# Kernel optimization log

Hardware: AMD Instinct MI355X
Metric: run time of the kernel (lower is better)

The kernel has to match this reference:

```python
import jax, jax.numpy as jnp
import numpy as np
from jax import lax

F = 64          # nb_filters
K_DOWN = 4      # size_kernel_sample
K_RES = 3       # size_kernel_res
DIL = 3         # rate_dilation_res
N_DOWN = 3      # downsampling blocks (one level)
N_RES = 4       # residual sub-blocks per block
N_EMB = 512     # codebook size
BETA = 0.25


def conv1d(x, w, b, stride=1, dil=1, act=True):
    # x: (B,T,C), w: (K,Cin,Cout)
    y = lax.conv_general_dilated(x, w, (stride,), 'SAME', rhs_dilation=(dil,),
                                 dimension_numbers=('NWC', 'WIO', 'NWC')) + b
    return jax.nn.relu(y) if act else y


def conv1d_t(x, w, b, stride):
    # transposed conv, w: (K, Cin, Cout)
    y = lax.conv_transpose(x, w, (stride,), 'SAME',
                           dimension_numbers=('NWC', 'WIO', 'NWC')) + b
    return jax.nn.relu(y)


def setup_inputs() -> dict:
    key = jax.random.key(0)
    ks = jax.random.split(key, 12)
    s_in = 1.0 / np.sqrt(K_DOWN * 1)
    s_f = 1.0 / np.sqrt(K_DOWN * F)
    s_r = 1.0 / np.sqrt(K_RES * F)
    return {
        'x': jax.random.normal(ks[0], (4, 65536, 1), dtype=jnp.float32),
        'w_down0': jax.random.normal(ks[1], (K_DOWN, 1, F), dtype=jnp.float32) * s_in,
        'b_down0': jnp.zeros((F,), jnp.float32),
        'w_down': jax.random.normal(ks[2], (N_DOWN - 1, K_DOWN, F, F), dtype=jnp.float32) * s_f,
        'b_down': jnp.zeros((N_DOWN - 1, F), jnp.float32),
        'w_res_enc': jax.random.normal(ks[3], (N_DOWN, N_RES, 2, K_RES, F, F), dtype=jnp.float32) * s_r,
        'b_res_enc': jnp.zeros((N_DOWN, N_RES, 2, F), jnp.float32),
        'codebook': jax.random.normal(ks[4], (N_EMB, F), dtype=jnp.float32),
        'w_res_dec': jax.random.normal(ks[5], (N_DOWN, N_RES, 2, K_RES, F, F), dtype=jnp.float32) * s_r,
        'b_res_dec': jnp.zeros((N_DOWN, N_RES, 2, F), jnp.float32),
        'w_up': jax.random.normal(ks[6], (N_DOWN, K_DOWN, F, F), dtype=jnp.float32) * s_f,
        'b_up': jnp.zeros((N_DOWN, F), jnp.float32),
        'w_proj': jax.random.normal(ks[7], (K_RES, F, 1), dtype=jnp.float32) * s_r,
        'b_proj': jnp.zeros((1,), jnp.float32),
    }


def reference(x, w_down0, b_down0, w_down, b_down, w_res_enc, b_res_enc,
              codebook, w_res_dec, b_res_dec, w_up, b_up, w_proj, b_proj):
    # ---- Encoder: N_DOWN stride-2 downsampling blocks, each followed by
    # N_RES ForwardResidualSubBlocks (dilated conv -> conv, residual add) ----
    h = conv1d(x, w_down0, b_down0, stride=2)
    for blk in range(N_DOWN):
        if blk > 0:
            h = conv1d(h, w_down[blk - 1], b_down[blk - 1], stride=2)
        for r in range(N_RES):
            y = conv1d(h, w_res_enc[blk, r, 0], b_res_enc[blk, r, 0], dil=DIL)
            y = conv1d(y, w_res_enc[blk, r, 1], b_res_enc[blk, r, 1], dil=1)
            h = h + y
    z_e = h  # (B, T/8, F)

    # ---- VectorQuantiser over channel axis ----
    dot = jnp.einsum('btd,kd->btk', z_e, codebook)          # tensordot
    nz = jnp.sum(jnp.square(z_e), axis=-1, keepdims=True)   # (B,T,1)
    ne = jnp.sum(jnp.square(codebook), axis=-1)             # (K,)
    dist = -2.0 * dot + nz + ne                             # squared cdist
    ids = jnp.argmin(dist, axis=-1)                         # (B,T)
    z_q = codebook[ids]                                     # embedding_lookup
    loss_commit = jnp.mean(jnp.linalg.norm(lax.stop_gradient(z_e) - z_q, axis=-1))
    loss_codebook = jnp.mean(jnp.linalg.norm(z_e - lax.stop_gradient(z_q), axis=-1))
    loss_vq = loss_codebook + BETA * loss_commit
    similarity = dot / jnp.sqrt(nz) / jnp.sqrt(ne)

    # ---- Decoder: residual blocks then stride-2 transposed conv, x N_DOWN ----
    h = z_q
    for blk in range(N_DOWN):
        for r in range(N_RES):
            y = conv1d(h, w_res_dec[blk, r, 0], b_res_dec[blk, r, 0], dil=1)
            y = conv1d(y, w_res_dec[blk, r, 1], b_res_dec[blk, r, 1], dil=DIL)
            h = h + y
        h = conv1d_t(h, w_up[blk], b_up[blk], stride=2)
    x_hat = conv1d(h, w_proj, b_proj, act=False)  # linear projection
    return x_hat, loss_vq, ids, similarity
```

## Files before the change

kernel.cpp:

```cpp
#include <hip/hip_runtime.h>
#include <cstdint>


#define OFF_LOSS 262144
#define OFF_IDS  262145
#define OFF_SIM  294913

__global__ __launch_bounds__(256) void down0_kernel(
    const float* __restrict__ x, const float* __restrict__ w,
    const float* __restrict__ bias, float* __restrict__ y)
{
  int idx = blockIdx.x * 256 + threadIdx.x;
  int co = idx & 63;
  int r  = idx >> 6;
  int t  = r & 32767;
  int b  = r >> 15;
  const float* xb = x + (size_t)b * 65536;
  float acc = bias[co];
  #pragma unroll
  for (int k = 0; k < 4; ++k) {
    int gt = 2 * t - 1 + k;
    float xv = ((unsigned)gt < 65536u) ? xb[gt] : 0.f;
    acc += xv * w[k * 64 + co];
  }
  y[(size_t)idx] = fmaxf(acc, 0.f);
}

template <int DIL, bool HAS_RES, int TT>
__global__ __launch_bounds__(512, 8) void conv3_kernel(
    const float* __restrict__ x, const float* __restrict__ w,
    const float* __restrict__ bias, const float* res,
    float* y, int T)
{
  constexpr int TPL = TT / 64;
  constexpr int XT  = TT + 2 * DIL;
  constexpr int XS0 = (XT + 3) & ~3;
  constexpr int XS  = (XS0 % 8 == 4) ? XS0 : XS0 + 4;
  constexpr int NV  = TPL + 2 * DIL;
  __shared__ float xs[64 * XS];
  const int tid  = threadIdx.x;
  const int lane = tid & 63;
  const int b    = blockIdx.y;
  const int t0   = blockIdx.x * TT;
  const int wv   = __builtin_amdgcn_readfirstlane(tid >> 6);
  const int co0  = __builtin_amdgcn_readfirstlane(wv * 8);

  const float* xb = x + (size_t)b * T * 64;
  for (int e = tid; e < 16 * XT; e += 512) {
    int tl = e >> 4, cq = (e & 15) * 4;
    int gt = t0 - DIL + tl;
    float4 v = make_float4(0.f, 0.f, 0.f, 0.f);
    if ((unsigned)gt < (unsigned)T) v = *(const float4*)&xb[(size_t)gt * 64 + cq];
    xs[(cq + 0) * XS + tl] = v.x;
    xs[(cq + 1) * XS + tl] = v.y;
    xs[(cq + 2) * XS + tl] = v.z;
    xs[(cq + 3) * XS + tl] = v.w;
  }
  __syncthreads();

  float acc[TPL][8] = {};
  const float* wb = w + co0;
  const int tb = TPL * lane;
  for (int ci = 0; ci < 64; ++ci) {
    const float* xr = xs + ci * XS + tb;
    float xv[NV];
    if constexpr (TPL == 2) {
      const float2* p2 = (const float2*)xr;
      #pragma unroll
      for (int q = 0; q < NV / 2; ++q) { float2 v = p2[q]; xv[2*q] = v.x; xv[2*q+1] = v.y; }
    } else {
      #pragma unroll
      for (int j = 0; j < NV; ++j) xv[j] = xr[j];
    }
    const float* w0 = wb + (0 * 64 + ci) * 64;
    const float* w1 = wb + (1 * 64 + ci) * 64;
    const float* w2 = wb + (2 * 64 + ci) * 64;
    #pragma unroll
    for (int j = 0; j < 8; ++j) {
      float c0 = w0[j], c1 = w1[j], c2 = w2[j];
      #pragma unroll
      for (int i = 0; i < TPL; ++i)
        acc[i][j] = fmaf(xv[i], c0, fmaf(xv[i + DIL], c1, fmaf(xv[i + 2 * DIL], c2, acc[i][j])));
    }
  }

  float bs[8];
  #pragma unroll
  for (int j = 0; j < 8; ++j) bs[j] = bias[co0 + j];
  #pragma unroll
  for (int i = 0; i < TPL; ++i) {
    size_t o = ((size_t)b * T + t0 + tb + i) * 64 + co0;
    float r[8];
    #pragma unroll
    for (int j = 0; j < 8; ++j) r[j] = fmaxf(acc[i][j] + bs[j], 0.f);
    if (HAS_RES) {
      float4 v0 = *(const float4*)&res[o];
      float4 v1 = *(const float4*)&res[o + 4];
      r[0] += v0.x; r[1] += v0.y; r[2] += v0.z; r[3] += v0.w;
      r[4] += v1.x; r[5] += v1.y; r[6] += v1.z; r[7] += v1.w;
    }
    *(float4*)&y[o]     = make_float4(r[0], r[1], r[2], r[3]);
    *(float4*)&y[o + 4] = make_float4(r[4], r[5], r[6], r[7]);
  }
}

__global__ __launch_bounds__(512, 8) void down2_kernel(
    const float* __restrict__ x, const float* __restrict__ w,
    const float* __restrict__ bias, float* __restrict__ y, int Tin)
{
  constexpr int XT = 130, XS = 132;
  __shared__ float xs[64 * XS];
  const int tid  = threadIdx.x;
  const int lane = tid & 63;
  const int b    = blockIdx.y;
  const int t0   = blockIdx.x * 64;
  const int Tout = Tin >> 1;
  const int wv   = __builtin_amdgcn_readfirstlane(tid >> 6);
  const int co0  = __builtin_amdgcn_readfirstlane(wv * 8);

  const float* xb = x + (size_t)b * Tin * 64;
  for (int e = tid; e < 16 * XT; e += 512) {
    int tl = e >> 4, cq = (e & 15) * 4;
    int gt = 2 * t0 - 1 + tl;
    float4 v = make_float4(0.f, 0.f, 0.f, 0.f);
    if ((unsigned)gt < (unsigned)Tin) v = *(const float4*)&xb[(size_t)gt * 64 + cq];
    xs[(cq + 0) * XS + tl] = v.x;
    xs[(cq + 1) * XS + tl] = v.y;
    xs[(cq + 2) * XS + tl] = v.z;
    xs[(cq + 3) * XS + tl] = v.w;
  }
  __syncthreads();

  float acc[8] = {};
  const float* wb = w + co0;
  for (int ci = 0; ci < 64; ++ci) {
    const float2* p2 = (const float2*)(xs + ci * XS + 2 * lane);
    float2 v0 = p2[0], v1 = p2[1];
    float a0 = v0.x, a1 = v0.y, a2 = v1.x, a3 = v1.y;
    const float* w0 = wb + (0 * 64 + ci) * 64;
    const float* w1 = wb + (1 * 64 + ci) * 64;
    const float* w2 = wb + (2 * 64 + ci) * 64;
    const float* w3 = wb + (3 * 64 + ci) * 64;
    #pragma unroll
    for (int j = 0; j < 8; ++j)
      acc[j] = fmaf(a0, w0[j], fmaf(a1, w1[j], fmaf(a2, w2[j], fmaf(a3, w3[j], acc[j]))));
  }

  size_t o = ((size_t)b * Tout + t0 + lane) * 64 + co0;
  #pragma unroll
  for (int q = 0; q < 2; ++q) {
    float4 rr;
    rr.x = fmaxf(acc[4*q+0] + bias[co0 + 4*q+0], 0.f);
    rr.y = fmaxf(acc[4*q+1] + bias[co0 + 4*q+1], 0.f);
    rr.z = fmaxf(acc[4*q+2] + bias[co0 + 4*q+2], 0.f);
    rr.w = fmaxf(acc[4*q+3] + bias[co0 + 4*q+3], 0.f);
    *(float4*)&y[o + 4 * q] = rr;
  }
}

__global__ __launch_bounds__(512, 8) void up_kernel(
    const float* __restrict__ x, const float* __restrict__ w,
    const float* __restrict__ bias, float* __restrict__ y, int Tin)
{
  constexpr int XT = 66, XS = 68;
  __shared__ float xs[64 * XS];
  const int tid  = threadIdx.x;
  const int lane = tid & 63;
  const int b    = blockIdx.y;
  const int u0   = blockIdx.x * 64;
  const int Tout = Tin << 1;
  const int wv   = __builtin_amdgcn_readfirstlane(tid >> 6);
  const int co0  = __builtin_amdgcn_readfirstlane(wv * 8);

  const float* xb = x + (size_t)b * Tin * 64;
  for (int e = tid; e < 16 * XT; e += 512) {
    int ul = e >> 4, cq = (e & 15) * 4;
    int gu = u0 - 1 + ul;
    float4 v = make_float4(0.f, 0.f, 0.f, 0.f);
    if ((unsigned)gu < (unsigned)Tin) v = *(const float4*)&xb[(size_t)gu * 64 + cq];
    xs[(cq + 0) * XS + ul] = v.x;
    xs[(cq + 1) * XS + ul] = v.y;
    xs[(cq + 2) * XS + ul] = v.z;
    xs[(cq + 3) * XS + ul] = v.w;
  }
  __syncthreads();

  float acce[8] = {}, acco[8] = {};
  const float* wb = w + co0;
  for (int ci = 0; ci < 64; ++ci) {
    const float* xr = xs + ci * XS + lane;
    float a0 = xr[0], a1 = xr[1], a2 = xr[2];
    const float* w0 = wb + (0 * 64 + ci) * 64;
    const float* w1 = wb + (1 * 64 + ci) * 64;
    const float* w2 = wb + (2 * 64 + ci) * 64;
    const float* w3 = wb + (3 * 64 + ci) * 64;
    #pragma unroll
    for (int j = 0; j < 8; ++j) {
      acce[j] = fmaf(a0, w0[j], fmaf(a1, w2[j], acce[j]));
      acco[j] = fmaf(a1, w1[j], fmaf(a2, w3[j], acco[j]));
    }
  }

  size_t oe = ((size_t)b * Tout + 2 * (u0 + lane)) * 64 + co0;
  size_t oo = oe + 64;
  #pragma unroll
  for (int q = 0; q < 2; ++q) {
    float4 re, ro;
    re.x = fmaxf(acce[4*q+0] + bias[co0 + 4*q+0], 0.f);
    re.y = fmaxf(acce[4*q+1] + bias[co0 + 4*q+1], 0.f);
    re.z = fmaxf(acce[4*q+2] + bias[co0 + 4*q+2], 0.f);
    re.w = fmaxf(acce[4*q+3] + bias[co0 + 4*q+3], 0.f);
    ro.x = fmaxf(acco[4*q+0] + bias[co0 + 4*q+0], 0.f);
    ro.y = fmaxf(acco[4*q+1] + bias[co0 + 4*q+1], 0.f);
    ro.z = fmaxf(acco[4*q+2] + bias[co0 + 4*q+2], 0.f);
    ro.w = fmaxf(acco[4*q+3] + bias[co0 + 4*q+3], 0.f);
    *(float4*)&y[oe + 4 * q] = re;
    *(float4*)&y[oo + 4 * q] = ro;
  }
}

__global__ __launch_bounds__(256) void proj_kernel(
    const float* __restrict__ x, const float* __restrict__ w,
    const float* __restrict__ bias, float* __restrict__ out)
{
  const int lane = threadIdx.x & 63;
  const int wid  = (blockIdx.x * 256 + threadIdx.x) >> 6;
  const float w0 = w[lane], w1 = w[64 + lane], w2 = w[128 + lane];
  const float bb = bias[0];
  size_t base = (size_t)wid * 64;
  for (int i = 0; i < 64; ++i) {
    size_t tau = base + i;
    int b = (int)(tau >> 16);
    int t = (int)(tau & 65535);
    const float* xb = x + ((size_t)b * 65536) * 64;
    float pm = (t > 0)     ? xb[(size_t)(t - 1) * 64 + lane] : 0.f;
    float pc =               xb[(size_t)t * 64 + lane];
    float pp = (t < 65535) ? xb[(size_t)(t + 1) * 64 + lane] : 0.f;
    float s = pm * w0 + pc * w1 + pp * w2;
    #pragma unroll
    for (int off = 32; off; off >>= 1) s += __shfl_down(s, off);
    if (lane == 0) out[tau] = s + bb;
  }
}

__global__ __launch_bounds__(256) void nz_kernel(
    const float* __restrict__ ze, float* __restrict__ nz)
{
  int lane = threadIdx.x & 63;
  int tok  = (blockIdx.x * 256 + threadIdx.x) >> 6;
  float v = ze[(size_t)tok * 64 + lane];
  float s = v * v;
  #pragma unroll
  for (int off = 32; off; off >>= 1) s += __shfl_down(s, off);
  if (lane == 0) nz[tok] = s;
}

#define VQA_TOKS 32
__global__ __launch_bounds__(256) void vq_dots_kernel(
    const float* __restrict__ ze, const float* __restrict__ cb,
    const float* __restrict__ nzbuf, float* __restrict__ sim_out,
    float2* __restrict__ pmin)
{
  __shared__ float zs[VQA_TOKS * 64];
  const int tid = threadIdx.x;
  {
    const float4* src = (const float4*)(ze + (size_t)blockIdx.x * VQA_TOKS * 64);
    float4* dst = (float4*)zs;
    dst[tid]       = src[tid];
    dst[tid + 256] = src[tid + 256];
  }
  const int c = blockIdx.y * 256 + tid;
  float r[64];
  #pragma unroll
  for (int q = 0; q < 16; ++q) {
    float4 a = ((const float4*)cb)[(size_t)c * 16 + q];
    r[4*q] = a.x; r[4*q+1] = a.y; r[4*q+2] = a.z; r[4*q+3] = a.w;
  }
  float ne = 0.f;
  #pragma unroll
  for (int d = 0; d < 64; ++d) ne += r[d] * r[d];
  const float rsne = 1.f / sqrtf(ne);
  const int wvid = tid >> 6;
  __syncthreads();

  for (int it = 0; it < VQA_TOKS; ++it) {
    const int tok = blockIdx.x * VQA_TOKS + it;
    const float4* z4 = (const float4*)(zs + it * 64);
    float dot = 0.f;
    #pragma unroll
    for (int q = 0; q < 16; ++q) {
      float4 zv = z4[q];
      dot += zv.x * r[4*q] + zv.y * r[4*q+1] + zv.z * r[4*q+2] + zv.w * r[4*q+3];
    }
    const float nzv = nzbuf[tok];
    float dist = (-2.f * dot + nzv) + ne;
    sim_out[(size_t)tok * 512 + c] = dot * (1.f / sqrtf(nzv)) * rsne;

    float md = dist; int mi = c;
    #pragma unroll
    for (int off = 32; off; off >>= 1) {
      float od = __shfl_down(md, off);
      int   oi = __shfl_down(mi, off);
      if (od < md || (od == md && oi < mi)) { md = od; mi = oi; }
    }
    if ((tid & 63) == 0) pmin[tok * 8 + blockIdx.y * 4 + wvid] = make_float2(md, (float)mi);
  }
}

__global__ __launch_bounds__(256) void vq_finish_kernel(
    const float* __restrict__ ze, const float* __restrict__ cb,
    const float2* __restrict__ pmin, float* __restrict__ zq,
    float* __restrict__ ids_out, float* __restrict__ blocksum)
{
  const int tid = threadIdx.x;
  const int lane = tid & 63, wvid = tid >> 6;
  float lloss = 0.f;
  for (int it = 0; it < 16; ++it) {
    const int tok = blockIdx.x * 64 + wvid * 16 + it;
    float bd = 1e30f; int bi = 0;
    #pragma unroll
    for (int p = 0; p < 8; ++p) {
      float2 pr = pmin[tok * 8 + p];
      float d = pr.x; int i = (int)pr.y;
      if (d < bd || (d == bd && i < bi)) { bd = d; bi = i; }
    }
    float zev = ze[(size_t)tok * 64 + lane];
    float cv  = cb[(size_t)bi * 64 + lane];
    float df = zev - cv;
    float s = df * df;
    #pragma unroll
    for (int off = 32; off; off >>= 1) s += __shfl_down(s, off);
    zq[(size_t)tok * 64 + lane] = cv;
    if (lane == 0) { ids_out[tok] = (float)bi; lloss += sqrtf(s); }
  }
  __shared__ float ls[4];
  if (lane == 0) ls[wvid] = lloss;
  __syncthreads();
  if (tid == 0) blocksum[blockIdx.x] = ls[0] + ls[1] + ls[2] + ls[3];
}

__global__ void loss_fin_kernel(const float* __restrict__ blocksum,
                                float* __restrict__ out)
{
  const int lane = threadIdx.x;
  float s = 0.f;
  for (int i = lane; i < 512; i += 64) s += blocksum[i];
  #pragma unroll
  for (int off = 32; off; off >>= 1) s += __shfl_down(s, off);
  if (lane == 0) out[0] = 1.25f * s / 32768.f;
}

#define LAUNCH_CONV3(DILV, RESV, XP, WP, BP, RP, YP)                           \
  do {                                                                         \
    if (T >= 16384)                                                            \
      conv3_kernel<DILV, RESV, 128><<<dim3(T / 128, 4), 512, 0, stream>>>(     \
          XP, WP, BP, RP, YP, T);                                              \
    else                                                                       \
      conv3_kernel<DILV, RESV, 64><<<dim3(T / 64, 4), 512, 0, stream>>>(       \
          XP, WP, BP, RP, YP, T);                                              \
  } while (0)

extern "C" void kernel_launch(void* const* d_in, const int* in_sizes, int n_in,
                              void* d_out, int out_size, void* d_ws, size_t ws_size,
                              hipStream_t stream)
{
  const float* x       = (const float*)d_in[0];
  const float* w_down0 = (const float*)d_in[1];
  const float* b_down0 = (const float*)d_in[2];
  const float* w_down  = (const float*)d_in[3];
  const float* b_down  = (const float*)d_in[4];
  const float* w_res_e = (const float*)d_in[5];
  const float* b_res_e = (const float*)d_in[6];
  const float* cb      = (const float*)d_in[7];
  const float* w_res_d = (const float*)d_in[8];
  const float* b_res_d = (const float*)d_in[9];
  const float* w_up    = (const float*)d_in[10];
  const float* b_up    = (const float*)d_in[11];
  const float* w_proj  = (const float*)d_in[12];
  const float* b_proj  = (const float*)d_in[13];

  float* out = (float*)d_out;
  const size_t BUF = (size_t)4 * 65536 * 64;
  float*  bufA     = (float*)d_ws;
  float*  bufB     = bufA + BUF;
  float*  nzbuf    = bufB + BUF;
  float2* pmin     = (float2*)(nzbuf + 32768);
  float*  blocksum = (float*)(pmin + 32768 * 8);

  float* h = bufA;
  float* tmp = bufB;

  down0_kernel<<<32768, 256, 0, stream>>>(x, w_down0, b_down0, h);
  int T = 32768;
  for (int blk = 0; blk < 3; ++blk) {
    if (blk > 0) {
      down2_kernel<<<dim3(T / 2 / 64, 4), 512, 0, stream>>>(
          h, w_down + (size_t)(blk - 1) * 4 * 64 * 64, b_down + (blk - 1) * 64, tmp, T);
      T >>= 1;
      float* s = h; h = tmp; tmp = s;
    }
    for (int r = 0; r < 4; ++r) {
      const float* w0p = w_res_e + (((size_t)blk * 4 + r) * 2 + 0) * 3 * 64 * 64;
      const float* w1p = w_res_e + (((size_t)blk * 4 + r) * 2 + 1) * 3 * 64 * 64;
      const float* b0p = b_res_e + (((size_t)blk * 4 + r) * 2 + 0) * 64;
      const float* b1p = b_res_e + (((size_t)blk * 4 + r) * 2 + 1) * 64;
      LAUNCH_CONV3(3, false, h, w0p, b0p, nullptr, tmp);
      LAUNCH_CONV3(1, true,  tmp, w1p, b1p, h, h);
    }
  }

  nz_kernel<<<8192, 256, 0, stream>>>(h, nzbuf);
  vq_dots_kernel<<<dim3(32768 / VQA_TOKS, 2), 256, 0, stream>>>(h, cb, nzbuf, out + OFF_SIM, pmin);
  vq_finish_kernel<<<512, 256, 0, stream>>>(h, cb, pmin, tmp, out + OFF_IDS, blocksum);
  loss_fin_kernel<<<1, 64, 0, stream>>>(blocksum, out + OFF_LOSS);
  { float* s = h; h = tmp; tmp = s; }

  for (int blk = 0; blk < 3; ++blk) {
    for (int r = 0; r < 4; ++r) {
      const float* w0p = w_res_d + (((size_t)blk * 4 + r) * 2 + 0) * 3 * 64 * 64;
      const float* w1p = w_res_d + (((size_t)blk * 4 + r) * 2 + 1) * 3 * 64 * 64;
      const float* b0p = b_res_d + (((size_t)blk * 4 + r) * 2 + 0) * 64;
      const float* b1p = b_res_d + (((size_t)blk * 4 + r) * 2 + 1) * 64;
      LAUNCH_CONV3(1, false, h, w0p, b0p, nullptr, tmp);
      LAUNCH_CONV3(3, true,  tmp, w1p, b1p, h, h);
    }
    up_kernel<<<dim3(2 * T / 128, 4), 512, 0, stream>>>(
        h, w_up + (size_t)blk * 4 * 64 * 64, b_up + blk * 64, tmp, T);
    T <<= 1;
    float* s = h; h = tmp; tmp = s;
  }

  proj_kernel<<<1024, 256, 0, stream>>>(h, w_proj, b_proj, out);
}
```

Measured before the change: 1.744 ms.

## Restructure VQ dot kernel to stream codebook and keep per-token accumulators

The VQ distance kernel now streams each codebook row in 16-float chunks and accumulates dots for all 32 tokens in registers, instead of holding the full 64-float codebook row in registers and looping over tokens. The per-token argmin drops the paired value/index shuffle reduction in favour of an fminf xor-reduction followed by a ballot to find the lowest matching lane. A launch-bounds occupancy hint of 6 is added. The aim is lower register pressure, higher occupancy and fewer shuffle instructions. The cost is 32 live accumulators and a different reduction order for the dot products, which could change argmin ties in rare cases.

Result: slower. 3.717 ms (+113.1%).

```diff
diff --git a/kernel.cpp b/kernel.cpp
--- a/kernel.cpp
+++ b/kernel.cpp
@@ -256,7 +256,7 @@
 }
 
 #define VQA_TOKS 32
-__global__ __launch_bounds__(256) void vq_dots_kernel(
+__global__ __launch_bounds__(256, 6) void vq_dots_kernel(
     const float* __restrict__ ze, const float* __restrict__ cb,
     const float* __restrict__ nzbuf, float* __restrict__ sim_out,
     float2* __restrict__ pmin)
@@ -270,40 +270,57 @@
     dst[tid + 256] = src[tid + 256];
   }
   const int c = blockIdx.y * 256 + tid;
-  float r[64];
-  #pragma unroll
-  for (int q = 0; q < 16; ++q) {
-    float4 a = ((const float4*)cb)[(size_t)c * 16 + q];
-    r[4*q] = a.x; r[4*q+1] = a.y; r[4*q+2] = a.z; r[4*q+3] = a.w;
-  }
+  const float4* cb4 = (const float4*)(cb + (size_t)c * 64);
+  const int wvid = tid >> 6;
+
+  float acc[VQA_TOKS];
+  #pragma unroll
+  for (int t = 0; t < VQA_TOKS; ++t) acc[t] = 0.f;
   float ne = 0.f;
-  #pragma unroll
-  for (int d = 0; d < 64; ++d) ne += r[d] * r[d];
+  __syncthreads();
+
+  #pragma unroll
+  for (int q = 0; q < 4; ++q) {
+    float4 w0 = cb4[4 * q + 0];
+    float4 w1 = cb4[4 * q + 1];
+    float4 w2 = cb4[4 * q + 2];
+    float4 w3 = cb4[4 * q + 3];
+    ne += w0.x * w0.x + w0.y * w0.y + w0.z * w0.z + w0.w * w0.w
+        + w1.x * w1.x + w1.y * w1.y + w1.z * w1.z + w1.w * w1.w
+        + w2.x * w2.x + w2.y * w2.y + w2.z * w2.z + w2.w * w2.w
+        + w3.x * w3.x + w3.y * w3.y + w3.z * w3.z + w3.w * w3.w;
+    const float4* zq4 = (const float4*)(zs + q * 16);
+    #pragma unroll
+    for (int t = 0; t < VQA_TOKS; ++t) {
+      float4 z0 = zq4[t * 16 + 0];
+      float4 z1 = zq4[t * 16 + 1];
+      float4 z2 = zq4[t * 16 + 2];
+      float4 z3 = zq4[t * 16 + 3];
+      acc[t] += z0.x * w0.x + z0.y * w0.y + z0.z * w0.z + z0.w * w0.w
+              + z1.x * w1.x + z1.y * w1.y + z1.z * w1.z + z1.w * w1.w
+              + z2.x * w2.x + z2.y * w2.y + z2.z * w2.z + z2.w * w2.w
+              + z3.x * w3.x + z3.y * w3.y + z3.z * w3.z + z3.w * w3.w;
+    }
+  }
   const float rsne = 1.f / sqrtf(ne);
-  const int wvid = tid >> 6;
-  __syncthreads();
-
-  for (int it = 0; it < VQA_TOKS; ++it) {
-    const int tok = blockIdx.x * VQA_TOKS + it;
-    const float4* z4 = (const float4*)(zs + it * 64);
-    float dot = 0.f;
-    #pragma unroll
-    for (int q = 0; q < 16; ++q) {
-      float4 zv = z4[q];
-      dot += zv.x * r[4*q] + zv.y * r[4*q+1] + zv.z * r[4*q+2] + zv.w * r[4*q+3];
-    }
+  const int cbase = blockIdx.y * 256 + wvid * 64;
+
+  #pragma unroll
+  for (int t = 0; t < VQA_TOKS; ++t) {
+    const int tok = blockIdx.x * VQA_TOKS + t;
     const float nzv = nzbuf[tok];
-    float dist = (-2.f * dot + nzv) + ne;
+    const float dot = acc[t];
+    const float dist = (-2.f * dot + nzv) + ne;
     sim_out[(size_t)tok * 512 + c] = dot * (1.f / sqrtf(nzv)) * rsne;
 
-    float md = dist; int mi = c;
-    #pragma unroll
-    for (int off = 32; off; off >>= 1) {
-      float od = __shfl_down(md, off);
-      int   oi = __shfl_down(mi, off);
-      if (od < md || (od == md && oi < mi)) { md = od; mi = oi; }
-    }
-    if ((tid & 63) == 0) pmin[tok * 8 + blockIdx.y * 4 + wvid] = make_float2(md, (float)mi);
+    float md = dist;
+    #pragma unroll
+    for (int off = 32; off; off >>= 1) md = fminf(md, __shfl_xor(md, off));
+    unsigned long long mk = __ballot(dist == md);
+    if ((tid & 63) == 0) {
+      int lmin = __ffsll(mk) - 1;
+      pmin[tok * 8 + blockIdx.y * 4 + wvid] = make_float2(md, (float)(cbase + lmin));
+    }
   }
 }
 
```

## Rewrite VQ distance kernel as register-tiled shared-memory GEMM

Applied to the files above, without the earlier changes.

Replaces the per-thread codebook-row-in-registers VQ dot kernel with a 64-token by 128-entry tiled GEMM. Both operands are staged transposed in shared memory and each thread computes a 4x8 register tile. Codebook norms move to a separate small kernel, and partial argmin results drop from 8 to 4 per token. The aim is higher FMA-to-load reuse in the distance and similarity stage and vectorized similarity stores. In exchange it adds one tiny launch and more shared memory per block.

Result: faster. 1.626 ms (-6.8%).

```diff
diff --git a/kernel.cpp b/kernel.cpp
--- a/kernel.cpp
+++ b/kernel.cpp
@@ -255,55 +255,109 @@
   if (lane == 0) nz[tok] = s;
 }
 
-#define VQA_TOKS 32
+__global__ __launch_bounds__(256) void ne_kernel(
+    const float* __restrict__ cb, float* __restrict__ ne)
+{
+  int c = blockIdx.x * 256 + threadIdx.x;
+  const float4* p = (const float4*)(cb + (size_t)c * 64);
+  float s = 0.f;
+  #pragma unroll
+  for (int q = 0; q < 16; ++q) {
+    float4 v = p[q];
+    s += v.x * v.x + v.y * v.y + v.z * v.z + v.w * v.w;
+  }
+  ne[c] = s;
+}
+
 __global__ __launch_bounds__(256) void vq_dots_kernel(
     const float* __restrict__ ze, const float* __restrict__ cb,
-    const float* __restrict__ nzbuf, float* __restrict__ sim_out,
-    float2* __restrict__ pmin)
-{
-  __shared__ float zs[VQA_TOKS * 64];
+    const float* __restrict__ nzbuf, const float* __restrict__ nebuf,
+    float* __restrict__ sim_out, float2* __restrict__ pmin)
+{
+  constexpr int ZS = 68, CS = 132;
+  __shared__ float zt[64 * ZS];
+  __shared__ float ct[64 * CS];
   const int tid = threadIdx.x;
+  const int tx  = tid & 15;
+  const int ty  = tid >> 4;
+  const int bx  = blockIdx.x, by = blockIdx.y;
+
   {
-    const float4* src = (const float4*)(ze + (size_t)blockIdx.x * VQA_TOKS * 64);
-    float4* dst = (float4*)zs;
-    dst[tid]       = src[tid];
-    dst[tid + 256] = src[tid + 256];
-  }
-  const int c = blockIdx.y * 256 + tid;
-  float r[64];
-  #pragma unroll
-  for (int q = 0; q < 16; ++q) {
-    float4 a = ((const float4*)cb)[(size_t)c * 16 + q];
-    r[4*q] = a.x; r[4*q+1] = a.y; r[4*q+2] = a.z; r[4*q+3] = a.w;
-  }
-  float ne = 0.f;
-  #pragma unroll
-  for (int d = 0; d < 64; ++d) ne += r[d] * r[d];
-  const float rsne = 1.f / sqrtf(ne);
-  const int wvid = tid >> 6;
+    const float* zb = ze + (size_t)bx * 64 * 64;
+    #pragma unroll
+    for (int it = 0; it < 4; ++it) {
+      int e = tid + it * 256;
+      int tl = e >> 4, cq = (e & 15) * 4;
+      float4 v = *(const float4*)&zb[tl * 64 + cq];
+      zt[(cq + 0) * ZS + tl] = v.x;
+      zt[(cq + 1) * ZS + tl] = v.y;
+      zt[(cq + 2) * ZS + tl] = v.z;
+      zt[(cq + 3) * ZS + tl] = v.w;
+    }
+    const float* cbb = cb + (size_t)by * 128 * 64;
+    #pragma unroll
+    for (int it = 0; it < 8; ++it) {
+      int e = tid + it * 256;
+      int el = e >> 4, cq = (e & 15) * 4;
+      float4 v = *(const float4*)&cbb[el * 64 + cq];
+      ct[(cq + 0) * CS + el] = v.x;
+      ct[(cq + 1) * CS + el] = v.y;
+      ct[(cq + 2) * CS + el] = v.z;
+      ct[(cq + 3) * CS + el] = v.w;
+    }
+  }
   __syncthreads();
 
-  for (int it = 0; it < VQA_TOKS; ++it) {
-    const int tok = blockIdx.x * VQA_TOKS + it;
-    const float4* z4 = (const float4*)(zs + it * 64);
-    float dot = 0.f;
-    #pragma unroll
-    for (int q = 0; q < 16; ++q) {
-      float4 zv = z4[q];
-      dot += zv.x * r[4*q] + zv.y * r[4*q+1] + zv.z * r[4*q+2] + zv.w * r[4*q+3];
-    }
-    const float nzv = nzbuf[tok];
-    float dist = (-2.f * dot + nzv) + ne;
-    sim_out[(size_t)tok * 512 + c] = dot * (1.f / sqrtf(nzv)) * rsne;
-
-    float md = dist; int mi = c;
-    #pragma unroll
-    for (int off = 32; off; off >>= 1) {
-      float od = __shfl_down(md, off);
-      int   oi = __shfl_down(mi, off);
+  float acc[4][8] = {};
+  #pragma unroll 4
+  for (int k = 0; k < 64; ++k) {
+    float4 zv = *(const float4*)&zt[k * ZS + ty * 4];
+    float4 c0 = *(const float4*)&ct[k * CS + tx * 8];
+    float4 c1 = *(const float4*)&ct[k * CS + tx * 8 + 4];
+    float zr[4] = {zv.x, zv.y, zv.z, zv.w};
+    float cr[8] = {c0.x, c0.y, c0.z, c0.w, c1.x, c1.y, c1.z, c1.w};
+    #pragma unroll
+    for (int i = 0; i < 4; ++i)
+      #pragma unroll
+      for (int j = 0; j < 8; ++j)
+        acc[i][j] = fmaf(zr[i], cr[j], acc[i][j]);
+  }
+
+  float4 nzq = *(const float4*)&nzbuf[bx * 64 + ty * 4];
+  float nzv[4] = {nzq.x, nzq.y, nzq.z, nzq.w};
+  float4 ne0  = *(const float4*)&nebuf[by * 128 + tx * 8];
+  float4 ne1  = *(const float4*)&nebuf[by * 128 + tx * 8 + 4];
+  float nev[8]  = {ne0.x, ne0.y, ne0.z, ne0.w, ne1.x, ne1.y, ne1.z, ne1.w};
+  float rsne[8];
+  #pragma unroll
+  for (int j = 0; j < 8; ++j) rsne[j] = 1.f / sqrtf(nev[j]);
+  const int ent0 = by * 128 + tx * 8;
+
+  #pragma unroll
+  for (int i = 0; i < 4; ++i) {
+    const int tok = bx * 64 + ty * 4 + i;
+    const float rsnz = 1.f / sqrtf(nzv[i]);
+    float dist[8], simv[8];
+    #pragma unroll
+    for (int j = 0; j < 8; ++j) {
+      dist[j] = (-2.f * acc[i][j] + nzv[i]) + nev[j];
+      simv[j] = acc[i][j] * rsnz * rsne[j];
+    }
+    float* so = sim_out + (size_t)tok * 512 + ent0;
+    *(float4*)&so[0] = make_float4(simv[0], simv[1], simv[2], simv[3]);
+    *(float4*)&so[4] = make_float4(simv[4], simv[5], simv[6], simv[7]);
+
+    float md = dist[0]; int mi = ent0;
+    #pragma unroll
+    for (int j = 1; j < 8; ++j)
+      if (dist[j] < md) { md = dist[j]; mi = ent0 + j; }
+    #pragma unroll
+    for (int off = 1; off < 16; off <<= 1) {
+      float od = __shfl_xor(md, off);
+      int   oi = __shfl_xor(mi, off);
       if (od < md || (od == md && oi < mi)) { md = od; mi = oi; }
     }
-    if ((tid & 63) == 0) pmin[tok * 8 + blockIdx.y * 4 + wvid] = make_float2(md, (float)mi);
+    if (tx == 0) pmin[tok * 4 + by] = make_float2(md, (float)mi);
   }
 }
 
@@ -319,8 +373,8 @@
     const int tok = blockIdx.x * 64 + wvid * 16 + it;
     float bd = 1e30f; int bi = 0;
     #pragma unroll
-    for (int p = 0; p < 8; ++p) {
-      float2 pr = pmin[tok * 8 + p];
+    for (int p = 0; p < 4; ++p) {
+      float2 pr = pmin[tok * 4 + p];
       float d = pr.x; int i = (int)pr.y;
       if (d < bd || (d == bd && i < bi)) { bd = d; bi = i; }
     }
@@ -384,8 +438,9 @@
   float*  bufA     = (float*)d_ws;
   float*  bufB     = bufA + BUF;
   float*  nzbuf    = bufB + BUF;
-  float2* pmin     = (float2*)(nzbuf + 32768);
-  float*  blocksum = (float*)(pmin + 32768 * 8);
+  float*  nebuf    = nzbuf + 32768;
+  float2* pmin     = (float2*)(nebuf + 512);
+  float*  blocksum = (float*)(pmin + 32768 * 4);
 
   float* h = bufA;
   float* tmp = bufB;
@@ -410,7 +465,8 @@
   }
 
   nz_kernel<<<8192, 256, 0, stream>>>(h, nzbuf);
-  vq_dots_kernel<<<dim3(32768 / VQA_TOKS, 2), 256, 0, stream>>>(h, cb, nzbuf, out + OFF_SIM, pmin);
+  ne_kernel<<<2, 256, 0, stream>>>(cb, nebuf);
+  vq_dots_kernel<<<dim3(512, 4), 256, 0, stream>>>(h, cb, nzbuf, nebuf, out + OFF_SIM, pmin);
   vq_finish_kernel<<<512, 256, 0, stream>>>(h, cb, pmin, tmp, out + OFF_IDS, blocksum);
   loss_fin_kernel<<<1, 64, 0, stream>>>(blocksum, out + OFF_LOSS);
   { float* s = h; h = tmp; tmp = s; }
```
